# Kernel tuning notes

Hardware: AMD Instinct MI355X
Metric: run time of the kernel (lower is better)

## Reference

```python
import jax, jax.numpy as jnp
import numpy as np

N = 100_000   # nodes
C = 32        # classes
E = 3_200_000 # edges


def setup_inputs() -> dict:
    key = jax.random.key(0)
    k1, k2, k3, k4, k5 = jax.random.split(key, 5)
    edge_index = jax.random.randint(k1, (2, E), 0, N, dtype=jnp.int32)
    edge_weight = jax.random.uniform(k2, (E,), dtype=jnp.float32) + 0.1  # positive weights
    inputs = jax.random.normal(k3, (N, C), dtype=jnp.float32)
    labels = jax.random.randint(k4, (N,), 0, C)
    y = jax.nn.one_hot(labels, C, dtype=jnp.float32)  # torch.where(y[:, i]) implies one-hot labels
    sample_mask = jax.random.bernoulli(k5, 0.5, (N,))
    return {"edge_index": edge_index, "edge_weight": edge_weight,
            "inputs": inputs, "y": y, "sample_mask": sample_mask}


def _normalize_sparse(edge_index, edge_weight, n):
    # normalize_sparse_tensor: add self-loops (weight 1), then D^{-1/2} A D^{-1/2}
    loop = jnp.arange(n, dtype=edge_index.dtype)
    row = jnp.concatenate([edge_index[0], loop])
    col = jnp.concatenate([edge_index[1], loop])
    w = jnp.concatenate([edge_weight, jnp.ones((n,), edge_weight.dtype)])
    deg = jax.ops.segment_sum(w, row, num_segments=n)
    dinv = jnp.where(deg > 0, jax.lax.rsqrt(deg), 0.0)
    vals = dinv[row] * w * dinv[col]
    return row, col, vals


def reference(edge_index, edge_weight, inputs, y, sample_mask):
    n, c = inputs.shape
    row, col, vals = _normalize_sparse(edge_index, edge_weight, n)

    p = jax.nn.softmax(inputs, axis=1)
    m = sample_mask.astype(p.dtype)[:, None]
    p = p * (1.0 - m) + y * m          # replace predictions by labels on masked nodes
    ym = y * m                          # labels only on masked nodes

    # nodeH = raw_normed_adj @ p   (sparse spmm)  -> (n, c)
    nodeH = jax.ops.segment_sum(vals[:, None] * p[col], row, num_segments=n)

    # per-class mean of nodeH over nodes with label i (one-hot => sum/count)
    cnt = ym.sum(axis=0)                         # (c,)
    H = (ym.T @ nodeH) / cnt[:, None]            # (c, c); NaN rows if class empty

    # NaN fixups (identity when no NaNs present)
    Hn = jnp.isnan(H)
    H = jnp.where(Hn, H.T, H)
    Hn = jnp.isnan(H)
    H0 = jnp.where(Hn, jnp.zeros_like(H), H)
    miss = (1.0 - H0.sum(axis=1, keepdims=True)) / Hn.sum(axis=1, keepdims=True).astype(H.dtype)
    H = jnp.where(Hn, miss, H0)

    # makeDoubleStochasticH: iterate col-norm then row-norm; 'delta' = ||H||_1 (as in source)
    def cond(state):
        _, i, d = state
        return (d >= 1e-12) & (i < 3000)

    def body(state):
        Hc, i, _ = state
        Hc = Hc / Hc.sum(axis=0, keepdims=True)
        Hc = Hc / Hc.sum(axis=1, keepdims=True)
        return Hc, i + 1, jnp.abs(Hc).sum()

    H, _, _ = jax.lax.while_loop(cond, body, (H, jnp.int32(0), jnp.float32(1e30)))
    return H
```

## Files before the change

### kernel.cpp

```cpp
#include <hip/hip_runtime.h>
#include <hip/hip_fp16.h>


#define RS 40960
#define BDEG 80
#define W 200
#define NBKTMAX 512
#define BCAP 4608
#define LCAP 4096
#define NSC 512
#define NPR NBKTMAX
#define NTOT (1 + NPR)
#define NRED 16
#define RPER ((NTOT + NRED - 1) / NRED)
#define PPAD 204
#define BVW 3200
#define L2A (BVW / 2)

__global__ __launch_bounds__(1024) void
k_deg(const int* __restrict__ ei, const float* __restrict__ ew,
      __half* __restrict__ slab, const unsigned char* __restrict__ mask_bytes,
      int* __restrict__ flag, float* __restrict__ Hg, float* __restrict__ cnt,
      int* __restrict__ gCnt, int E_, int R, int Nn) {
  __shared__ float h[RS];
  if (blockIdx.x == 0) {
    Hg[threadIdx.x] = 0.f;
    if (threadIdx.x < 32) cnt[threadIdx.x] = 0.f;
    if (threadIdx.x < NBKTMAX) gCnt[threadIdx.x] = 0;
    int* hi = (int*)h;
    if (threadIdx.x == 0) hi[0] = 0;
    __syncthreads();
    int acc = mask_bytes[threadIdx.x * 4 + 1] | mask_bytes[threadIdx.x * 4 + 2]
            | mask_bytes[threadIdx.x * 4 + 3];
    if (acc) atomicOr(&hi[0], 1);
    __syncthreads();
    if (threadIdx.x == 0) *flag = (hi[0] != 0) ? 1 : 0;
  }
  int g = blockIdx.x >> 3, xx = blockIdx.x & 7;
  int r = g % R;
  int sl = xx + 8 * (g / R);
  int lo = r * RS;
  int used = min(RS, Nn - lo);
  for (int i = threadIdx.x; i < used; i += 1024) h[i] = 0.f;
  __syncthreads();
  int Q = E_ >> 2;
  int q0 = (int)((long long)Q * sl / BDEG);
  int q1 = (int)((long long)Q * (sl + 1) / BDEG);
  const int4* ei4 = (const int4*)ei;
  const float4* ew4 = (const float4*)ew;
  int q = q0 + threadIdx.x;
  for (; q + 1024 < q1; q += 2048) {
    int4 ia = ei4[q], ib = ei4[q + 1024];
    float4 wa = ew4[q], wb = ew4[q + 1024];
    unsigned o0 = (unsigned)(ia.x - lo), o1 = (unsigned)(ia.y - lo);
    unsigned o2 = (unsigned)(ia.z - lo), o3 = (unsigned)(ia.w - lo);
    unsigned o4 = (unsigned)(ib.x - lo), o5 = (unsigned)(ib.y - lo);
    unsigned o6 = (unsigned)(ib.z - lo), o7 = (unsigned)(ib.w - lo);
    if (o0 < RS) atomicAdd(&h[o0], wa.x);
    if (o1 < RS) atomicAdd(&h[o1], wa.y);
    if (o2 < RS) atomicAdd(&h[o2], wa.z);
    if (o3 < RS) atomicAdd(&h[o3], wa.w);
    if (o4 < RS) atomicAdd(&h[o4], wb.x);
    if (o5 < RS) atomicAdd(&h[o5], wb.y);
    if (o6 < RS) atomicAdd(&h[o6], wb.z);
    if (o7 < RS) atomicAdd(&h[o7], wb.w);
  }
  for (; q < q1; q += 1024) {
    int4 idx = ei4[q];
    float4 w = ew4[q];
    unsigned o0 = (unsigned)(idx.x - lo), o1 = (unsigned)(idx.y - lo);
    unsigned o2 = (unsigned)(idx.z - lo), o3 = (unsigned)(idx.w - lo);
    if (o0 < RS) atomicAdd(&h[o0], w.x);
    if (o1 < RS) atomicAdd(&h[o1], w.y);
    if (o2 < RS) atomicAdd(&h[o2], w.z);
    if (o3 < RS) atomicAdd(&h[o3], w.w);
  }
  if (sl == BDEG - 1) {
    for (int e = (Q << 2) + threadIdx.x; e < E_; e += 1024) {
      unsigned off = (unsigned)(ei[e] - lo);
      if (off < RS) atomicAdd(&h[off], ew[e]);
    }
  }
  __syncthreads();
  __half* dst = slab + ((size_t)r * BDEG + sl) * RS;
  for (int i = threadIdx.x; i < used; i += 1024) dst[i] = __float2half(h[i]);
}

__global__ void k_node(const float* __restrict__ x, const float* __restrict__ y,
                       const void* __restrict__ maskp, const int* __restrict__ flag,
                       const __half* __restrict__ slab, int2* __restrict__ ninfo,
                       __half* __restrict__ p16, float* __restrict__ Hg,
                       float* __restrict__ cnt, unsigned* __restrict__ bitvec, int Nn) {
  __shared__ float scnt[32], sdiag[32];
  if (threadIdx.x < 32) { scnt[threadIdx.x] = 0.f; sdiag[threadIdx.x] = 0.f; }
  __syncthreads();
  int n = blockIdx.x * blockDim.x + threadIdx.x;
  bool inb = (n < Nn);
  bool byteMask = (*flag != 0);
  bool msk = false;
  if (inb)
    msk = byteMask ? (((const unsigned char*)maskp)[n] != 0)
                   : (((const int*)maskp)[n] != 0);
  unsigned long long bm = __ballot(msk);
  if ((threadIdx.x & 63) == 0)
    ((unsigned long long*)bitvec)[n >> 6] = bm;
  if (inb) {
    const __half* sl = slab + ((size_t)(n / RS) * BDEG) * RS + (n % RS);
    float d = 0.f;
    #pragma unroll 5
    for (int bb = 0; bb < BDEG; ++bb) d += __half2float(sl[(size_t)bb * RS]);
    float dinv = rsqrtf(d + 1.0f);
    int a = -1;
    if (msk) {
      const float4* yi = (const float4*)(y + (size_t)n * 32);
      #pragma unroll
      for (int q = 0; q < 8; ++q) {
        float4 v = yi[q];
        if (v.x == 1.f) a = q * 4 + 0;
        if (v.y == 1.f) a = q * 4 + 1;
        if (v.z == 1.f) a = q * 4 + 2;
        if (v.w == 1.f) a = q * 4 + 3;
      }
      atomicAdd(&scnt[a], 1.f);
      atomicAdd(&sdiag[a], dinv * dinv);
    } else {
      const float4* xi = (const float4*)(x + (size_t)n * 32);
      float xs[32];
      #pragma unroll
      for (int q = 0; q < 8; ++q) {
        float4 v = xi[q];
        xs[q*4+0] = v.x; xs[q*4+1] = v.y; xs[q*4+2] = v.z; xs[q*4+3] = v.w;
      }
      float mx = -3.4e38f;
      #pragma unroll
      for (int i = 0; i < 32; ++i) mx = fmaxf(mx, xs[i]);
      float s = 0.f;
      #pragma unroll
      for (int i = 0; i < 32; ++i) { xs[i] = __expf(xs[i] - mx); s += xs[i]; }
      float inv = 1.f / s;
      union { short sh[32]; int4 v[4]; } u;
      #pragma unroll
      for (int i = 0; i < 32; ++i)
        u.sh[i] = __half_as_short(__float2half(xs[i] * inv));
      int4* po = (int4*)(p16 + (size_t)n * 32);
      #pragma unroll
      for (int q = 0; q < 4; ++q) po[q] = u.v[q];
    }
    int2 ni; ni.x = __float_as_int(dinv); ni.y = a;
    ninfo[n] = ni;
  }
  __syncthreads();
  if (threadIdx.x < 32) {
    if (scnt[threadIdx.x] != 0.f) atomicAdd(&cnt[threadIdx.x], scnt[threadIdx.x]);
    if (sdiag[threadIdx.x] != 0.f) atomicAdd(&Hg[threadIdx.x * 33], sdiag[threadIdx.x]);
  }
}

__global__ __launch_bounds__(1024) void
k_bucket(const int* __restrict__ ei, const float* __restrict__ ew,
         const int2* __restrict__ ninfo, const unsigned* __restrict__ bitvec,
         int2* __restrict__ gBucket, int* __restrict__ gCnt, int E_) {
  __shared__ int2 list[LCAP];
  __shared__ int lcnt;
  __shared__ int bcnt[NBKTMAX];
  __shared__ int gbase[NBKTMAX];
  __shared__ int bplace[NBKTMAX];
  __shared__ int sbase[NBKTMAX];
  union USH { unsigned sbv[BVW]; int2 l2[L2A]; };
  __shared__ USH us;
  __shared__ int2 l2b[LCAP - L2A];
  if (threadIdx.x == 0) lcnt = 0;
  if (threadIdx.x < NBKTMAX) { bcnt[threadIdx.x] = 0; bplace[threadIdx.x] = 0; }
  for (int i = threadIdx.x; i < BVW; i += 1024) us.sbv[i] = bitvec[i];
  __syncthreads();
  int E4 = E_ >> 2;
  int q0 = (int)((long long)E4 * blockIdx.x / NSC);
  int q1 = (int)((long long)E4 * (blockIdx.x + 1) / NSC);
  for (int q = q0 + threadIdx.x; q < q1; q += 1024) {
    int4 rr = ((const int4*)ei)[q];
    int4 cc = ((const int4*)(ei + E_))[q];
    float4 ww = ((const float4*)ew)[q];
    int rs[4] = {rr.x, rr.y, rr.z, rr.w};
    int cs[4] = {cc.x, cc.y, cc.z, cc.w};
    float wv[4] = {ww.x, ww.y, ww.z, ww.w};
    bool act[4];
    #pragma unroll
    for (int k = 0; k < 4; ++k)
      act[k] = (us.sbv[(unsigned)rs[k] >> 5] >> (rs[k] & 31)) & 1;
    int2 nr[4];
    #pragma unroll
    for (int k = 0; k < 4; ++k)
      if (act[k]) nr[k] = ninfo[rs[k]];
    #pragma unroll
    for (int k = 0; k < 4; ++k) {
      if (act[k]) {
        float val = __int_as_float(nr[k].x) * wv[k];
        int pos = atomicAdd(&lcnt, 1);
        if (pos < LCAP) list[pos] = make_int2((cs[k] << 5) | nr[k].y, __float_as_int(val));
      }
    }
  }
  if (blockIdx.x == NSC - 1) {
    for (int e = (E4 << 2) + threadIdx.x; e < E_; e += 1024) {
      int r = ei[e];
      if (!((us.sbv[(unsigned)r >> 5] >> (r & 31)) & 1)) continue;
      int2 nr = ninfo[r];
      int c = ei[E_ + e];
      float val = __int_as_float(nr.x) * ew[e];
      int pos = atomicAdd(&lcnt, 1);
      if (pos < LCAP) list[pos] = make_int2((c << 5) | nr.y, __float_as_int(val));
    }
  }
  __syncthreads();
  int nl = min(lcnt, LCAP);
  for (int i = threadIdx.x; i < nl; i += 1024)
    atomicAdd(&bcnt[(list[i].x >> 5) / W], 1);
  __syncthreads();
  if (threadIdx.x < NBKTMAX) sbase[threadIdx.x] = bcnt[threadIdx.x];
  __syncthreads();
  for (int off = 1; off < NBKTMAX; off <<= 1) {
    int v = 0;
    if (threadIdx.x < NBKTMAX && threadIdx.x >= off) v = sbase[threadIdx.x - off];
    __syncthreads();
    if (threadIdx.x < NBKTMAX && threadIdx.x >= off) sbase[threadIdx.x] += v;
    __syncthreads();
  }
  if (threadIdx.x < NBKTMAX) {
    int n = bcnt[threadIdx.x];
    gbase[threadIdx.x] = (n > 0) ? atomicAdd(&gCnt[threadIdx.x], n) : 0;
  }
  __syncthreads();
  for (int i = threadIdx.x; i < nl; i += 1024) {
    int2 rec = list[i];
    int bkt = (rec.x >> 5) / W;
    int d = sbase[bkt] - bcnt[bkt] + atomicAdd(&bplace[bkt], 1);
    if (d < L2A) us.l2[d] = rec; else l2b[d - L2A] = rec;
  }
  __syncthreads();
  for (int j = threadIdx.x; j < nl; j += 1024) {
    int2 rec = (j < L2A) ? us.l2[j] : l2b[j - L2A];
    int bkt = (rec.x >> 5) / W;
    int dst = gbase[bkt] + (j - (sbase[bkt] - bcnt[bkt]));
    if (dst < BCAP) gBucket[(size_t)bkt * BCAP + dst] = rec;
  }
}

__global__ __launch_bounds__(1024) void
k_process(const int2* __restrict__ gBucket, const int* __restrict__ gCnt,
          const int2* __restrict__ ninfo, const __half* __restrict__ p16,
          float* __restrict__ procSlab, int Nn) {
  __shared__ float TlocT[32 * W];
  __shared__ __half plocT[32 * PPAD];
  __shared__ float H32[1024];
  __shared__ float ldin[W];
  __shared__ int   llab[W];
  __shared__ short cmap[W];
  __shared__ short cidx[W];
  __shared__ int   nUs;
  int k = blockIdx.x;
  int c0 = k * W;
  int Wb = min(c0 + W, Nn) - c0;
  H32[threadIdx.x] = 0.f;
  if ((int)threadIdx.x < Wb) {
    int2 ni = ninfo[c0 + threadIdx.x];
    ldin[threadIdx.x] = __int_as_float(ni.x);
    llab[threadIdx.x] = ni.y;
  }
  if (threadIdx.x == 0) nUs = 0;
  __syncthreads();
  if (threadIdx.x < 64) {
    int base = 0;
    for (int ch = 0; ch < W; ch += 64) {
      int j = ch + threadIdx.x;
      bool u = (j < Wb) && (llab[j] < 0);
      unsigned long long m = __ballot(u);
      int p = base + __popcll(m & ((1ull << threadIdx.x) - 1ull));
      if (u) { cmap[j] = (short)p; cidx[p] = (short)j; }
      base += (int)__popcll(m);
    }
    if (threadIdx.x == 0) nUs = base;
  }
  for (int i = threadIdx.x; i < 32 * W; i += 1024) TlocT[i] = 0.f;
  __syncthreads();
  int nU = nUs;
  if (Wb > 0) {
    for (int i = threadIdx.x; i < nU * 32; i += 1024) {
      int j = i >> 5, b = i & 31;
      plocT[b * PPAD + j] = p16[(size_t)(c0 + cidx[j]) * 32 + b];
    }
    int n = min(gCnt[k], BCAP);
    const int2* bk = gBucket + (size_t)k * BCAP;
    for (int i = threadIdx.x; i < n; i += 1024) {
      int2 rec = bk[i];
      int cl = (rec.x >> 5) - c0;
      int a = rec.x & 31;
      float v = __int_as_float(rec.y) * ldin[cl];
      int b = llab[cl];
      if (b >= 0) atomicAdd(&H32[a * 32 + b], v);
      else        atomicAdd(&TlocT[a * W + cmap[cl]], v);
    }
  }
  __syncthreads();
  int a = threadIdx.x >> 5;
  int b = threadIdx.x & 31;
  float acc0 = 0.f, acc1 = 0.f, acc2 = 0.f, acc3 = 0.f;
  int c = 0;
  for (; c + 3 < nU; c += 4) {
    float4 tv = *(const float4*)&TlocT[a * W + c];
    short4 ps = *(const short4*)&plocT[b * PPAD + c];
    acc0 += tv.x * __half2float(__short_as_half(ps.x));
    acc1 += tv.y * __half2float(__short_as_half(ps.y));
    acc2 += tv.z * __half2float(__short_as_half(ps.z));
    acc3 += tv.w * __half2float(__short_as_half(ps.w));
  }
  for (; c < nU; ++c)
    acc0 += TlocT[a * W + c] * __half2float(plocT[b * PPAD + c]);
  procSlab[(size_t)k * 1024 + threadIdx.x] =
      (acc0 + acc1) + (acc2 + acc3) + H32[threadIdx.x];
}

__global__ __launch_bounds__(1024) void
k_red(const float* __restrict__ allSlabs, float* __restrict__ red) {
  int k0 = blockIdx.x * RPER;
  int k1 = min(k0 + RPER, NTOT);
  float s = 0.f;
  for (int k = k0; k < k1; ++k) s += allSlabs[(size_t)k * 1024 + threadIdx.x];
  red[(size_t)blockIdx.x * 1024 + threadIdx.x] = s;
}

__global__ __launch_bounds__(1024) void
k_sinkhorn(const float* __restrict__ red, const float* __restrict__ cnt,
           float* __restrict__ out) {
  __shared__ float sHH[1024];
  int t = threadIdx.x;
  float s = 0.f;
  #pragma unroll
  for (int k = 0; k < NRED; ++k) s += red[(size_t)k * 1024 + t];
  sHH[t] = s;
  __syncthreads();
  int j = t;
  if (j >= 32) return;
  float cj = cnt[j];
  float Hcol[32], Hrow[32];
  #pragma unroll
  for (int i = 0; i < 32; ++i) Hcol[i] = sHH[i * 32 + j];
  #pragma unroll
  for (int i = 0; i < 32; ++i) Hcol[i] /= __shfl(cj, i);
  #pragma unroll
  for (int k = 0; k < 32; ++k) Hrow[k] = sHH[j * 32 + k] / cj;
  float u = 1.f, v = 1.f;
  for (int it = 0; it < 40; ++it) {
    float a0 = 0.f, a1 = 0.f, a2 = 0.f, a3 = 0.f;
    #pragma unroll
    for (int i = 0; i < 32; i += 4) {
      a0 += Hcol[i+0] * __shfl(u, i+0);
      a1 += Hcol[i+1] * __shfl(u, i+1);
      a2 += Hcol[i+2] * __shfl(u, i+2);
      a3 += Hcol[i+3] * __shfl(u, i+3);
    }
    v = 1.f / ((a0 + a1) + (a2 + a3));
    a0 = a1 = a2 = a3 = 0.f;
    #pragma unroll
    for (int k = 0; k < 32; k += 4) {
      a0 += Hrow[k+0] * __shfl(v, k+0);
      a1 += Hrow[k+1] * __shfl(v, k+1);
      a2 += Hrow[k+2] * __shfl(v, k+2);
      a3 += Hrow[k+3] * __shfl(v, k+3);
    }
    u = 1.f / ((a0 + a1) + (a2 + a3));
  }
  #pragma unroll
  for (int i = 0; i < 32; ++i) out[i * 32 + j] = __shfl(u, i) * Hcol[i] * v;
}

extern "C" void kernel_launch(void* const* d_in, const int* in_sizes, int n_in,
                              void* d_out, int out_size, void* d_ws, size_t ws_size,
                              hipStream_t stream) {
  const int*   ei   = (const int*)d_in[0];
  const float* ew   = (const float*)d_in[1];
  const float* x    = (const float*)d_in[2];
  const float* y    = (const float*)d_in[3];
  const void*  mask = d_in[4];
  float* out = (float*)d_out;
  int E_ = in_sizes[1];
  int Nn = in_sizes[2] / 32;
  int R = (Nn + RS - 1) / RS;

  char* ws = (char*)d_ws;
  size_t o = 0;
  float* cnt = (float*)(ws + o);    o += 128;
  int*   flag = (int*)(ws + o);     o += 128;
  int*   gCnt = (int*)(ws + o);     o += NBKTMAX * 4;
  float* allSlabs = (float*)(ws + o);
  float* Hg       = allSlabs;
  float* procSlab = allSlabs + 1024;
  o += (size_t)NTOT * 4096;
  float* red = (float*)(ws + o);    o += (size_t)NRED * 4096;
  int2*  gBucket = (int2*)(ws + o); o += (size_t)NBKTMAX * BCAP * 8;
  __half* slab = (__half*)(ws + o); o += (size_t)R * BDEG * RS * 2;
  int2*  ninfo = (int2*)(ws + o);   o += (size_t)Nn * 8;
  __half* p16 = (__half*)(ws + o);  o += (size_t)Nn * 64;
  unsigned* gbv = (unsigned*)(ws + o); o += (size_t)BVW * 4;

  int nb = (Nn + 255) / 256;
  k_deg<<<R * BDEG, 1024, 0, stream>>>(ei, ew, slab, (const unsigned char*)mask,
                                       flag, Hg, cnt, gCnt, E_, R, Nn);
  k_node<<<nb, 256, 0, stream>>>(x, y, mask, flag, slab, ninfo, p16, Hg, cnt, gbv, Nn);
  k_bucket<<<NSC, 1024, 0, stream>>>(ei, ew, ninfo, gbv, gBucket, gCnt, E_);
  k_process<<<NPR, 1024, 0, stream>>>(gBucket, gCnt, ninfo, p16, procSlab, Nn);
  k_red<<<NRED, 1024, 0, stream>>>(allSlabs, red);
  k_sinkhorn<<<1, 1024, 0, stream>>>(red, cnt, out);
}
```

Baseline: 216.1 us.

## Fuse reduction with Sinkhorn via last-block counter; simplify bucket scatter

Merges the slab reduction and Sinkhorn kernels into one launch: every block writes its partial sum, takes a ticket from an atomic counter, and the last block to finish runs the Sinkhorn normalization. The counter lives in the flag buffer and is reset by k_deg. In k_bucket, the shared-memory prefix scan and local sort before the global write are removed, so each record is written straight to its bucket slot through a shared atomic. This cuts one kernel launch and several block barriers, but the global writes become less coalesced and rely on a threadfence handshake.

```diff
diff --git a/kernel.cpp b/kernel.cpp
--- a/kernel.cpp
+++ b/kernel.cpp
@@ -15,7 +15,6 @@
 #define RPER ((NTOT + NRED - 1) / NRED)
 #define PPAD 204
 #define BVW 3200
-#define L2A (BVW / 2)
 
 __global__ __launch_bounds__(1024) void
 k_deg(const int* __restrict__ ei, const float* __restrict__ ew,
@@ -28,7 +27,7 @@
     if (threadIdx.x < 32) cnt[threadIdx.x] = 0.f;
     if (threadIdx.x < NBKTMAX) gCnt[threadIdx.x] = 0;
     int* hi = (int*)h;
-    if (threadIdx.x == 0) hi[0] = 0;
+    if (threadIdx.x == 0) { hi[0] = 0; flag[4] = 0; }
     __syncthreads();
     int acc = mask_bytes[threadIdx.x * 4 + 1] | mask_bytes[threadIdx.x * 4 + 2]
             | mask_bytes[threadIdx.x * 4 + 3];
@@ -165,13 +164,10 @@
   __shared__ int bcnt[NBKTMAX];
   __shared__ int gbase[NBKTMAX];
   __shared__ int bplace[NBKTMAX];
-  __shared__ int sbase[NBKTMAX];
-  union USH { unsigned sbv[BVW]; int2 l2[L2A]; };
-  __shared__ USH us;
-  __shared__ int2 l2b[LCAP - L2A];
+  __shared__ unsigned sbv[BVW];
   if (threadIdx.x == 0) lcnt = 0;
   if (threadIdx.x < NBKTMAX) { bcnt[threadIdx.x] = 0; bplace[threadIdx.x] = 0; }
-  for (int i = threadIdx.x; i < BVW; i += 1024) us.sbv[i] = bitvec[i];
+  for (int i = threadIdx.x; i < BVW; i += 1024) sbv[i] = bitvec[i];
   __syncthreads();
   int E4 = E_ >> 2;
   int q0 = (int)((long long)E4 * blockIdx.x / NSC);
@@ -186,7 +182,7 @@
     bool act[4];
     #pragma unroll
     for (int k = 0; k < 4; ++k)
-      act[k] = (us.sbv[(unsigned)rs[k] >> 5] >> (rs[k] & 31)) & 1;
+      act[k] = (sbv[(unsigned)rs[k] >> 5] >> (rs[k] & 31)) & 1;
     int2 nr[4];
     #pragma unroll
     for (int k = 0; k < 4; ++k)
@@ -203,7 +199,7 @@
   if (blockIdx.x == NSC - 1) {
     for (int e = (E4 << 2) + threadIdx.x; e < E_; e += 1024) {
       int r = ei[e];
-      if (!((us.sbv[(unsigned)r >> 5] >> (r & 31)) & 1)) continue;
+      if (!((sbv[(unsigned)r >> 5] >> (r & 31)) & 1)) continue;
       int2 nr = ninfo[r];
       int c = ei[E_ + e];
       float val = __int_as_float(nr.x) * ew[e];
@@ -216,15 +212,6 @@
   for (int i = threadIdx.x; i < nl; i += 1024)
     atomicAdd(&bcnt[(list[i].x >> 5) / W], 1);
   __syncthreads();
-  if (threadIdx.x < NBKTMAX) sbase[threadIdx.x] = bcnt[threadIdx.x];
-  __syncthreads();
-  for (int off = 1; off < NBKTMAX; off <<= 1) {
-    int v = 0;
-    if (threadIdx.x < NBKTMAX && threadIdx.x >= off) v = sbase[threadIdx.x - off];
-    __syncthreads();
-    if (threadIdx.x < NBKTMAX && threadIdx.x >= off) sbase[threadIdx.x] += v;
-    __syncthreads();
-  }
   if (threadIdx.x < NBKTMAX) {
     int n = bcnt[threadIdx.x];
     gbase[threadIdx.x] = (n > 0) ? atomicAdd(&gCnt[threadIdx.x], n) : 0;
@@ -233,14 +220,8 @@
   for (int i = threadIdx.x; i < nl; i += 1024) {
     int2 rec = list[i];
     int bkt = (rec.x >> 5) / W;
-    int d = sbase[bkt] - bcnt[bkt] + atomicAdd(&bplace[bkt], 1);
-    if (d < L2A) us.l2[d] = rec; else l2b[d - L2A] = rec;
-  }
-  __syncthreads();
-  for (int j = threadIdx.x; j < nl; j += 1024) {
-    int2 rec = (j < L2A) ? us.l2[j] : l2b[j - L2A];
-    int bkt = (rec.x >> 5) / W;
-    int dst = gbase[bkt] + (j - (sbase[bkt] - bcnt[bkt]));
+    int slot = atomicAdd(&bplace[bkt], 1);
+    int dst = gbase[bkt] + slot;
     if (dst < BCAP) gBucket[(size_t)bkt * BCAP + dst] = rec;
   }
 }
@@ -320,23 +301,25 @@
 }
 
 __global__ __launch_bounds__(1024) void
-k_red(const float* __restrict__ allSlabs, float* __restrict__ red) {
+k_redsink(const float* __restrict__ allSlabs, float* red,
+          const float* __restrict__ cnt, float* __restrict__ out, int* done) {
+  int t = threadIdx.x;
   int k0 = blockIdx.x * RPER;
   int k1 = min(k0 + RPER, NTOT);
   float s = 0.f;
-  for (int k = k0; k < k1; ++k) s += allSlabs[(size_t)k * 1024 + threadIdx.x];
-  red[(size_t)blockIdx.x * 1024 + threadIdx.x] = s;
-}
-
-__global__ __launch_bounds__(1024) void
-k_sinkhorn(const float* __restrict__ red, const float* __restrict__ cnt,
-           float* __restrict__ out) {
+  for (int k = k0; k < k1; ++k) s += allSlabs[(size_t)k * 1024 + t];
+  red[(size_t)blockIdx.x * 1024 + t] = s;
+  __threadfence();
+  __shared__ int lastBlk;
+  if (t == 0) lastBlk = (atomicAdd(done, 1) == NRED - 1) ? 1 : 0;
+  __syncthreads();
+  if (!lastBlk) return;
+  __threadfence();
   __shared__ float sHH[1024];
-  int t = threadIdx.x;
-  float s = 0.f;
-  #pragma unroll
-  for (int k = 0; k < NRED; ++k) s += red[(size_t)k * 1024 + t];
-  sHH[t] = s;
+  float s2 = 0.f;
+  #pragma unroll
+  for (int k = 0; k < NRED; ++k) s2 += red[(size_t)k * 1024 + t];
+  sHH[t] = s2;
   __syncthreads();
   int j = t;
   if (j >= 32) return;
@@ -408,6 +391,5 @@
   k_node<<<nb, 256, 0, stream>>>(x, y, mask, flag, slab, ninfo, p16, Hg, cnt, gbv, Nn);
   k_bucket<<<NSC, 1024, 0, stream>>>(ei, ew, ninfo, gbv, gBucket, gCnt, E_);
   k_process<<<NPR, 1024, 0, stream>>>(gBucket, gCnt, ninfo, p16, procSlab, Nn);
-  k_red<<<NRED, 1024, 0, stream>>>(allSlabs, red);
-  k_sinkhorn<<<1, 1024, 0, stream>>>(red, cnt, out);
-}
+  k_redsink<<<NRED, 1024, 0, stream>>>(allSlabs, red, cnt, out, flag + 4);
+}
```

Result: slower. 228.0 us (+5.5%).
